# Optimization experiments

Hardware: AMD Instinct MI355X
Metric: run time of the kernel (lower is better)

Reference implementation:

```python
import jax, jax.numpy as jnp
import numpy as np

NEG_SLOPE = 0.01  # torch leaky_relu default
EPS = 1e-12      # torch F.normalize default


def _edge_mlp(edge_attr, w1, b1, w2, b2, d_h):
    # Sequential(Linear, ReLU, Linear) -> per-edge weight matrices [E, d_h, d_h]
    h = jax.nn.relu(edge_attr @ w1 + b1)
    return (h @ w2 + b2).reshape(-1, d_h, d_h)


def _nnconv(h, src, dst, w_edge, root, bias, n_nodes):
    # message_j->i = x_j @ Theta(e_ji); aggregate (add) at dst; add root transform + bias
    msg = jnp.einsum('ei,eio->eo', h[src], w_edge)  # [E, d_h]
    agg = jax.ops.segment_sum(msg, dst, num_segments=n_nodes)
    return agg + h @ root + bias


def setup_inputs() -> dict:
    key = jax.random.key(0)
    ks = jax.random.split(key, 20)
    N, E, G = 20000, 200000, 128
    d_node, d_edge, d_h, d_out = 64, 16, 32, 32

    x = jax.random.normal(ks[0], (N, d_node), dtype=jnp.float32)
    edge_index = jax.random.randint(ks[1], (2, E), 0, N, dtype=jnp.int32)
    edge_attr = jax.random.normal(ks[2], (E, d_edge), dtype=jnp.float32)
    batch = jnp.sort(jax.random.randint(ks[3], (N,), 0, G, dtype=jnp.int32))

    def lin(k, fan_in, fan_out):
        kw, kb = jax.random.split(k)
        s = 1.0 / np.sqrt(fan_in)
        w = jax.random.uniform(kw, (fan_in, fan_out), jnp.float32, -s, s)
        b = jax.random.uniform(kb, (fan_out,), jnp.float32, -s, s)
        return w, b

    nfc_w, nfc_b = lin(ks[4], d_node, d_h)
    efc1_w1, efc1_b1 = lin(ks[5], d_edge, d_h)
    efc1_w2, efc1_b2 = lin(ks[6], d_h, d_h * d_h)
    root1 = jax.random.uniform(ks[7], (d_h, d_h), jnp.float32, -1/np.sqrt(d_h), 1/np.sqrt(d_h))
    bias1 = jnp.zeros((d_h,), jnp.float32)
    efc2_w1, efc2_b1 = lin(ks[8], d_edge, d_h)
    efc2_w2, efc2_b2 = lin(ks[9], d_h, d_h * d_h)
    root2 = jax.random.uniform(ks[10], (d_h, d_h), jnp.float32, -1/np.sqrt(d_h), 1/np.sqrt(d_h))
    bias2 = jnp.zeros((d_h,), jnp.float32)
    fc_w, fc_b = lin(ks[11], d_h, d_out)

    return dict(x=x, edge_index=edge_index, edge_attr=edge_attr, batch=batch,
                num_graphs=G,
                nfc_w=nfc_w, nfc_b=nfc_b,
                efc1_w1=efc1_w1, efc1_b1=efc1_b1, efc1_w2=efc1_w2, efc1_b2=efc1_b2,
                root1=root1, bias1=bias1,
                efc2_w1=efc2_w1, efc2_b1=efc2_b1, efc2_w2=efc2_w2, efc2_b2=efc2_b2,
                root2=root2, bias2=bias2,
                fc_w=fc_w, fc_b=fc_b)


def reference(x, edge_index, edge_attr, batch, num_graphs,
              nfc_w, nfc_b,
              efc1_w1, efc1_b1, efc1_w2, efc1_b2, root1, bias1,
              efc2_w1, efc2_b1, efc2_w2, efc2_b2, root2, bias2,
              fc_w, fc_b):
    n_nodes = x.shape[0]
    d_h = nfc_w.shape[1]
    src, dst = edge_index[0], edge_index[1]

    lrelu = lambda v: jax.nn.leaky_relu(v, NEG_SLOPE)
    # dropout(p=0.1) is identity at inference
    h = lrelu(x @ nfc_w + nfc_b)

    w_e1 = _edge_mlp(edge_attr, efc1_w1, efc1_b1, efc1_w2, efc1_b2, d_h)
    h = lrelu(_nnconv(h, src, dst, w_e1, root1, bias1, n_nodes))

    w_e2 = _edge_mlp(edge_attr, efc2_w1, efc2_b1, efc2_w2, efc2_b2, d_h)
    atom_embs = lrelu(_nnconv(h, src, dst, w_e2, root2, bias2, n_nodes))

    pooled = jax.ops.segment_sum(atom_embs, batch, num_segments=num_graphs)  # [G, d_h]
    norm = jnp.linalg.norm(pooled, ord=2, axis=1, keepdims=True)
    pooled = pooled / jnp.maximum(norm, EPS)

    out = pooled @ fc_w + fc_b
    return (out, atom_embs)
```

## Files before the change

### kernel.cpp

```cpp
#include <hip/hip_runtime.h>
#include <stdint.h>

#define NN 20000
#define NE 200000
#define NG 128
#define NWJOBS 3125
#define EGRID 782
#define L2SLICE 819

typedef __attribute__((ext_vector_type(8))) short short8;
typedef __attribute__((ext_vector_type(4))) float f32x4;
typedef __attribute__((ext_vector_type(4))) int   int4v;
typedef __attribute__((ext_vector_type(2))) unsigned int uint2v;

static __device__ __forceinline__ float bf2f(short s) {
    union { unsigned int u; float f; } x;
    x.u = ((unsigned int)(unsigned short)s) << 16;
    return x.f;
}
static __device__ __forceinline__ unsigned short f2bf(float f) {
    unsigned int u = __builtin_bit_cast(unsigned int, f);
    u += 0x7fffu + ((u >> 16) & 1u);
    return (unsigned short)(u >> 16);
}
static __device__ __forceinline__ unsigned int pack2bf(float a, float b) {
    unsigned int u0 = __builtin_bit_cast(unsigned int, a) + 0x8000u;
    unsigned int u1 = __builtin_bit_cast(unsigned int, b) + 0x8000u;
    return __builtin_amdgcn_perm(u1, u0, 0x07060302u);
}
static __device__ __forceinline__ int detect_isbf(const unsigned int* x) {
    unsigned int u = x[threadIdx.x & 63];
    unsigned int el = (u >> 7) & 0xffu;
    unsigned long long bm = __ballot((el >= 100u) && (el <= 140u));
    return __popcll(bm) > 32;
}

__global__ __launch_bounds__(256) void k_prep_all(
    const void* x, const void* nfcw, const void* nfcb,
    const void* root1, const void* bias1,
    const void* w2a, const void* b2a, const void* w2b, const void* b2b,
    const void* w1a, const void* b1a, const void* w1b, const void* b1b,
    const void* ea,
    float* __restrict__ h0, float* __restrict__ aggA, float* __restrict__ aggB,
    short* __restrict__ W2Ta, short* __restrict__ W2Tb,
    short* __restrict__ w1t_ws, float* __restrict__ b1f_ws,
    short* __restrict__ ea_ws) {
    const int isbf = detect_isbf((const unsigned int*)x);
    const int b = blockIdx.x;

    if (b < 2500) {
        __shared__ float wf[64 * 32];
        __shared__ float rf[32 * 32];
        __shared__ float bfs[32];
        __shared__ float rb[32];
        __shared__ float xrow[8][66];
        __shared__ float hrow[8][33];
        for (int i = threadIdx.x; i < 64 * 32; i += 256)
            wf[i] = isbf ? bf2f(((const short*)nfcw)[i]) : ((const float*)nfcw)[i];
        for (int i = threadIdx.x; i < 32 * 32; i += 256)
            rf[i] = isbf ? bf2f(((const short*)root1)[i]) : ((const float*)root1)[i];
        if (threadIdx.x < 32) {
            bfs[threadIdx.x] = isbf ? bf2f(((const short*)nfcb)[threadIdx.x])
                                    : ((const float*)nfcb)[threadIdx.x];
            rb[threadIdx.x]  = isbf ? bf2f(((const short*)bias1)[threadIdx.x])
                                    : ((const float*)bias1)[threadIdx.x];
        }
        int t = b * 256 + threadIdx.x;
        int v = t >> 5, c = t & 31, vl = threadIdx.x >> 5;
        if (isbf) {
            const short* xr = (const short*)x + (size_t)v * 64;
            xrow[vl][c]      = bf2f(xr[c]);
            xrow[vl][32 + c] = bf2f(xr[32 + c]);
        } else {
            const float* xr = (const float*)x + (size_t)v * 64;
            xrow[vl][c]      = xr[c];
            xrow[vl][32 + c] = xr[32 + c];
        }
        __syncthreads();
        float acc = bfs[c];
#pragma unroll
        for (int q = 0; q < 64; ++q) acc += xrow[vl][q] * wf[q * 32 + c];
        float hv = acc > 0.f ? acc : 0.01f * acc;
        h0[t] = hv;
        hrow[vl][c] = hv;
        __syncthreads();
        float a2 = rb[c];
#pragma unroll
        for (int q = 0; q < 32; ++q) a2 += hrow[vl][q] * rf[q * 32 + c];
        aggA[t] = a2;
        return;
    }
    if (b < 4327) {
        const int bb = b - 2500;
        if (bb == 1) {
            for (int i = threadIdx.x; i < 1024; i += 256) {
                int layer = i >> 9, jj = i & 511, c = jj >> 4, q = jj & 15;
                const void* w1p = layer ? w1b : w1a;
                w1t_ws[i] = isbf ? ((const short*)w1p)[q * 32 + c]
                                 : (short)f2bf(((const float*)w1p)[q * 32 + c]);
            }
            for (int i = threadIdx.x; i < 64; i += 256) {
                int layer = i >> 5, c = i & 31;
                const void* b1p = layer ? b1b : b1a;
                b1f_ws[i] = isbf ? bf2f(((const short*)b1p)[c])
                                 : ((const float*)b1p)[c];
            }
        }
        int t = bb * 256 + threadIdx.x;
        if (t < 2 * 32 * 1056) {
            int layer = t / (32 * 1056);
            int r = t - layer * (32 * 1056);
            int o = r / 1056, kp = r - o * 1056;
            const void* w2 = layer ? w2b : w2a;
            const void* b2 = layer ? b2b : b2a;
            int idx; const void* sp;
            if (kp < 1024) { int kk = kp >> 5, i = kp & 31; idx = kk * 1024 + i * 32 + o; sp = w2; }
            else           { int i = kp - 1024;             idx = i * 32 + o;             sp = b2; }
            short v = isbf ? ((const short*)sp)[idx] : (short)f2bf(((const float*)sp)[idx]);
            (layer ? W2Tb : W2Ta)[o * 1056 + kp] = v;
            return;
        }
        int u = t - 2 * 32 * 1056;
        if (u < NE * 2 && !isbf) {
            const float* p = (const float*)ea + (size_t)u * 8;
            f32x4 f0 = *(const f32x4*)p;
            f32x4 f1 = *(const f32x4*)(p + 4);
            union { unsigned int d[4]; short8 v; } o8;
            o8.d[0] = pack2bf(f0[0], f0[1]);
            o8.d[1] = pack2bf(f0[2], f0[3]);
            o8.d[2] = pack2bf(f1[0], f1[1]);
            o8.d[3] = pack2bf(f1[2], f1[3]);
            *(short8*)&ea_ws[(size_t)u * 8] = o8.v;
        }
        return;
    }
    {
        int idx = (b - 4327) * 256 + threadIdx.x;
        if (idx < NN * 32 / 4) {
            f32x4 z = {0.f, 0.f, 0.f, 0.f};
            ((f32x4*)aggB)[idx] = z;
        }
    }
}

__global__ __launch_bounds__(256, 4) void k_edge(
    const float* __restrict__ h_in,
    const short* __restrict__ W2T,
    const short* __restrict__ w1pre,
    const float* __restrict__ b1pre,
    const int* __restrict__ src, const int* __restrict__ dst,
    const short* __restrict__ ea_bf,
    const short* __restrict__ ea_ws,
    const unsigned int* xdet,
    float* agg,
    const int layer2, const void* rootp, const void* biasp) {
    __shared__ __align__(16) short h1l[4 * 32 * 68];

    const int isbf = detect_isbf(xdet);
    const short* eap = isbf ? ea_bf : ea_ws;

    if (layer2) {
        const int base = blockIdx.x * L2SLICE;
        for (int i = threadIdx.x; i < L2SLICE; i += 256) {
            int t = base + i;
            if (t < NN * 32) {
                int v = t >> 5, c = t & 31;
                const float* ar = h_in + (size_t)v * 32;
                float acc = isbf ? bf2f(((const short*)biasp)[c]) : ((const float*)biasp)[c];
#pragma unroll
                for (int q = 0; q < 32; ++q) {
                    float hv = ar[q];
                    hv = hv > 0.f ? hv : 0.01f * hv;
                    float wv = isbf ? bf2f(((const short*)rootp)[q * 32 + c])
                                    : ((const float*)rootp)[q * 32 + c];
                    acc += hv * wv;
                }
                atomicAdd(&agg[t], acc);
            }
        }
    }

    const int lane = threadIdx.x & 63;
    const int wid  = threadIdx.x >> 6;
    const int m    = lane & 15;
    const int quad = lane >> 4;
    const int wb   = wid * (32 * 68);

    const int w = blockIdx.x * 4 + wid;
    if (w >= NWJOBS) return;

    short8 w1lo = {0, 0, 0, 0, 0, 0, 0, 0};
    short8 w1hi = {0, 0, 0, 0, 0, 0, 0, 0};
    if (quad < 2) {
        w1lo = *(const short8*)&w1pre[m * 16 + ((quad & 1) << 3)];
        w1hi = *(const short8*)&w1pre[(m + 16) * 16 + ((quad & 1) << 3)];
    }
    const float b1lo = b1pre[m];
    const float b1hi = b1pre[m + 16];
    const f32x4 zero4 = {0.f, 0.f, 0.f, 0.f};

    const int e0 = w << 6;
    short8 eafc[4];
    f32x4 hs[4][2];
    int4v dv[4];
    {
        int s0[4];
#pragma unroll
        for (int mt = 0; mt < 4; ++mt) {
            eafc[mt] = *(const short8*)&eap[(size_t)(e0 + mt * 16 + m) * 16 + ((quad & 1) << 3)];
            s0[mt] = src[e0 + mt * 16 + m];
            dv[mt] = *(const int4v*)&dst[e0 + mt * 16 + (quad << 2)];
        }
#pragma unroll
        for (int mt = 0; mt < 4; ++mt) {
            const float* hr = h_in + (size_t)s0[mt] * 32 + (quad << 3);
            hs[mt][0] = *(const f32x4*)hr;
            hs[mt][1] = *(const f32x4*)(hr + 4);
        }
    }

#pragma unroll
    for (int mt = 0; mt < 4; ++mt) {
        f32x4 alo = __builtin_amdgcn_mfma_f32_16x16x32_bf16(eafc[mt], w1lo, zero4, 0, 0, 0);
        f32x4 ahi = __builtin_amdgcn_mfma_f32_16x16x32_bf16(eafc[mt], w1hi, zero4, 0, 0, 0);
        float v0 = fmaxf(alo[0] + b1lo, 0.f);
        float v1 = fmaxf(alo[1] + b1lo, 0.f);
        float v2 = fmaxf(alo[2] + b1lo, 0.f);
        float v3 = fmaxf(alo[3] + b1lo, 0.f);
        uint2v dlo; dlo[0] = pack2bf(v0, v1); dlo[1] = pack2bf(v2, v3);
        *(uint2v*)&h1l[wb + m * 68 + (mt << 4) + (quad << 2)] = dlo;
        v0 = fmaxf(ahi[0] + b1hi, 0.f);
        v1 = fmaxf(ahi[1] + b1hi, 0.f);
        v2 = fmaxf(ahi[2] + b1hi, 0.f);
        v3 = fmaxf(ahi[3] + b1hi, 0.f);
        uint2v dhi; dhi[0] = pack2bf(v0, v1); dhi[1] = pack2bf(v2, v3);
        *(uint2v*)&h1l[wb + (m + 16) * 68 + (mt << 4) + (quad << 2)] = dhi;
    }
    __asm volatile("s_waitcnt lgkmcnt(0)" ::: "memory");

    short8 hsbf[4];
#pragma unroll
    for (int mt = 0; mt < 4; ++mt) {
        f32x4 g0 = hs[mt][0], g1 = hs[mt][1];
        if (layer2) {
#pragma unroll
            for (int p = 0; p < 4; ++p) {
                g0[p] = g0[p] > 0.f ? g0[p] : 0.01f * g0[p];
                g1[p] = g1[p] > 0.f ? g1[p] : 0.01f * g1[p];
            }
        }
        union { unsigned int du[4]; short8 v; } a;
        a.du[0] = pack2bf(g0[0], g0[1]);
        a.du[1] = pack2bf(g0[2], g0[3]);
        a.du[2] = pack2bf(g1[0], g1[1]);
        a.du[3] = pack2bf(g1[2], g1[3]);
        hsbf[mt] = a.v;
    }

    const short* wr0 = W2T + m * 1056 + (quad << 3);
    const short* wr1 = W2T + (m + 16) * 1056 + (quad << 3);
    f32x4 acc0[4] = {zero4, zero4, zero4, zero4};
    f32x4 acc1[4] = {zero4, zero4, zero4, zero4};
    short8 q0[4], q1[4];
#pragma unroll
    for (int p = 0; p < 4; ++p) {
        q0[p] = *(const short8*)(wr0 + (p << 5));
        q1[p] = *(const short8*)(wr1 + (p << 5));
    }
#pragma unroll
    for (int s = 0; s < 33; ++s) {
        short8 bf0 = q0[s & 3];
        short8 bf1 = q1[s & 3];
        if (s + 4 < 33) {
            q0[s & 3] = *(const short8*)(wr0 + ((s + 4) << 5));
            q1[s & 3] = *(const short8*)(wr1 + ((s + 4) << 5));
        }
        if (s < 32) {
#pragma unroll
            for (int mt = 0; mt < 4; ++mt) {
                uint2v hd = *(const uint2v*)&h1l[wb + s * 68 + (mt << 4) + (quad << 2)];
                f32x4 hv;
                hv[0] = __builtin_bit_cast(float, hd[0] << 16);
                hv[1] = __builtin_bit_cast(float, hd[0] & 0xffff0000u);
                hv[2] = __builtin_bit_cast(float, hd[1] << 16);
                hv[3] = __builtin_bit_cast(float, hd[1] & 0xffff0000u);
                f32x4 u0 = __builtin_amdgcn_mfma_f32_16x16x32_bf16(hsbf[mt], bf0, zero4, 0, 0, 0);
                f32x4 u1 = __builtin_amdgcn_mfma_f32_16x16x32_bf16(hsbf[mt], bf1, zero4, 0, 0, 0);
                acc0[mt] += hv * u0;
                acc1[mt] += hv * u1;
            }
        } else {
#pragma unroll
            for (int mt = 0; mt < 4; ++mt) {
                acc0[mt] = __builtin_amdgcn_mfma_f32_16x16x32_bf16(hsbf[mt], bf0, acc0[mt], 0, 0, 0);
                acc1[mt] = __builtin_amdgcn_mfma_f32_16x16x32_bf16(hsbf[mt], bf1, acc1[mt], 0, 0, 0);
            }
        }
    }

#pragma unroll
    for (int mt = 0; mt < 4; ++mt) {
#pragma unroll
        for (int r = 0; r < 4; ++r) {
            float* ap = agg + (size_t)dv[mt][r] * 32 + m;
            atomicAdd(ap, acc0[mt][r]);
            atomicAdd(ap + 16, acc1[mt][r]);
        }
    }
}

__global__ __launch_bounds__(256) void k_final(
    const float* __restrict__ agg, const int* __restrict__ batch,
    const unsigned int* xdet, void* __restrict__ out,
    const void* fcw, const void* fcb) {
    const int isbf = detect_isbf(xdet);
    const int g = blockIdx.x;
    __shared__ int srange[2];
    __shared__ float gacc[8][32];
    __shared__ float pn[32];
    if (threadIdx.x < 2) {
        int target = g + (int)threadIdx.x;
        int lo = 0, hi = NN;
        while (lo < hi) {
            int mid = (lo + hi) >> 1;
            if (batch[mid] < target) lo = mid + 1; else hi = mid;
        }
        srange[threadIdx.x] = lo;
    }
    __syncthreads();
    const int ns = srange[0], ne = srange[1];
    const int c = threadIdx.x & 31;
    float psum = 0.f;
    for (int idx = ns * 32 + threadIdx.x; idx < ne * 32; idx += 256) {
        float v = agg[idx];
        v = v > 0.f ? v : 0.01f * v;
        if (isbf) ((short*)out)[4096 + idx] = (short)f2bf(v);
        else      ((float*)out)[4096 + idx] = v;
        psum += v;
    }
    gacc[threadIdx.x >> 5][c] = psum;
    __syncthreads();
    if (threadIdx.x < 32) {
        float p = 0.f;
#pragma unroll
        for (int r = 0; r < 8; ++r) p += gacc[r][threadIdx.x];
        float sq = p * p;
#pragma unroll
        for (int o = 16; o > 0; o >>= 1) sq += __shfl_xor(sq, o, 64);
        float inv = 1.0f / fmaxf(sqrtf(sq), 1e-12f);
        pn[threadIdx.x] = p * inv;
    }
    __syncthreads();
    if (threadIdx.x < 32) {
        const int t = threadIdx.x;
        float acc = isbf ? bf2f(((const short*)fcb)[t]) : ((const float*)fcb)[t];
#pragma unroll
        for (int q = 0; q < 32; ++q) {
            float wv = isbf ? bf2f(((const short*)fcw)[q * 32 + t])
                            : ((const float*)fcw)[q * 32 + t];
            acc += pn[q] * wv;
        }
        if (isbf) ((short*)out)[g * 32 + t] = (short)f2bf(acc);
        else      ((float*)out)[g * 32 + t] = acc;
    }
}

extern "C" void kernel_launch(void* const* d_in, const int* in_sizes, int n_in,
                              void* d_out, int out_size, void* d_ws, size_t ws_size,
                              hipStream_t stream) {
    (void)in_sizes; (void)n_in; (void)out_size; (void)ws_size;
    const void* x     = d_in[0];
    const int*  eidx  = (const int*)d_in[1];
    const void* ea    = d_in[2];
    const int*  batch = (const int*)d_in[3];
    const void* nfcw  = d_in[5];
    const void* nfcb  = d_in[6];
    const void* e1w1  = d_in[7];
    const void* e1b1  = d_in[8];
    const void* e1w2  = d_in[9];
    const void* e1b2  = d_in[10];
    const void* root1 = d_in[11];
    const void* bias1 = d_in[12];
    const void* e2w1  = d_in[13];
    const void* e2b1  = d_in[14];
    const void* e2w2  = d_in[15];
    const void* e2b2  = d_in[16];
    const void* root2 = d_in[17];
    const void* bias2 = d_in[18];
    const void* fcw   = d_in[19];
    const void* fcb   = d_in[20];
    const unsigned int* xdet = (const unsigned int*)x;

    char* ws = (char*)d_ws;
    float* h0     = (float*)ws; ws += (size_t)NN * 32 * 4;
    float* aggA   = (float*)ws; ws += (size_t)NN * 32 * 4;
    float* aggB   = (float*)ws; ws += (size_t)NN * 32 * 4;
    short* W2T1   = (short*)ws; ws += 32 * 1056 * 2;
    short* W2T2   = (short*)ws; ws += 32 * 1056 * 2;
    short* w1t_ws = (short*)ws; ws += 1024 * 2;
    float* b1f_ws = (float*)ws; ws += 64 * 4;
    short* ea_ws  = (short*)ws; ws += (size_t)NE * 16 * 2;

    const int* srcp = eidx;
    const int* dstp = eidx + NE;

    k_prep_all<<<4952, 256, 0, stream>>>(
        x, nfcw, nfcb, root1, bias1,
        e1w2, e1b2, e2w2, e2b2, e1w1, e1b1, e2w1, e2b1, ea,
        h0, aggA, aggB, W2T1, W2T2, w1t_ws, b1f_ws, ea_ws);

    k_edge<<<EGRID, 256, 0, stream>>>(h0, W2T1, w1t_ws, b1f_ws, srcp, dstp,
                                      (const short*)ea, ea_ws, xdet, aggA,
                                      0, nullptr, nullptr);
    k_edge<<<EGRID, 256, 0, stream>>>(aggA, W2T2, w1t_ws + 512, b1f_ws + 32, srcp, dstp,
                                      (const short*)ea, ea_ws, xdet, aggB,
                                      1, root2, bias2);
    k_final<<<NG, 256, 0, stream>>>(aggB, batch, xdet, d_out, fcw, fcb);
}
```

Measured before the change: 218.5 us.

## Stage edge-MLP second-layer weights in LDS and use 1024-thread persistent blocks

The edge kernel now launches 256 blocks of 1024 threads. Each block first copies the transposed second-layer weight matrix (about 66KB in bf16) into shared memory with a padded row stride. The inner MFMA loop then reads B fragments from LDS instead of prefetching them from global or L2 memory into registers. Wave jobs are strided across blocks, and the layer-2 root transform is split into 2500-element slices per block. This cuts global weight traffic and register pressure, but it raises LDS use per block to roughly 135KB, leaves only one block per CU, adds a block-wide barrier, and wave count per block caps occupancy.

Measured after the change: 196.2 us. 10.2% less time.

```diff
diff --git a/kernel.cpp b/kernel.cpp
--- a/kernel.cpp
+++ b/kernel.cpp
@@ -5,8 +5,7 @@
 #define NE 200000
 #define NG 128
 #define NWJOBS 3125
-#define EGRID 782
-#define L2SLICE 819
+#define EBLK 256
 
 typedef __attribute__((ext_vector_type(8))) short short8;
 typedef __attribute__((ext_vector_type(4))) float f32x4;
@@ -143,7 +142,7 @@
     }
 }
 
-__global__ __launch_bounds__(256, 4) void k_edge(
+__global__ __launch_bounds__(1024, 4) void k_edge(
     const float* __restrict__ h_in,
     const short* __restrict__ W2T,
     const short* __restrict__ w1pre,
@@ -154,31 +153,35 @@
     const unsigned int* xdet,
     float* agg,
     const int layer2, const void* rootp, const void* biasp) {
-    __shared__ __align__(16) short h1l[4 * 32 * 68];
+    __shared__ __align__(16) short w2t[32 * 1058];
+    __shared__ __align__(16) short h1l[16 * 32 * 68];
 
     const int isbf = detect_isbf(xdet);
     const short* eap = isbf ? ea_bf : ea_ws;
 
+    for (int c = threadIdx.x; c < 32 * 132; c += 1024) {
+        int o = c / 132, t8 = c - o * 132;
+        *(short8*)&w2t[o * 1058 + (t8 << 3)] = *(const short8*)&W2T[o * 1056 + (t8 << 3)];
+    }
     if (layer2) {
-        const int base = blockIdx.x * L2SLICE;
-        for (int i = threadIdx.x; i < L2SLICE; i += 256) {
+        const int base = blockIdx.x * 2500;
+        for (int i = threadIdx.x; i < 2500; i += 1024) {
             int t = base + i;
-            if (t < NN * 32) {
-                int v = t >> 5, c = t & 31;
-                const float* ar = h_in + (size_t)v * 32;
-                float acc = isbf ? bf2f(((const short*)biasp)[c]) : ((const float*)biasp)[c];
-#pragma unroll
-                for (int q = 0; q < 32; ++q) {
-                    float hv = ar[q];
-                    hv = hv > 0.f ? hv : 0.01f * hv;
-                    float wv = isbf ? bf2f(((const short*)rootp)[q * 32 + c])
-                                    : ((const float*)rootp)[q * 32 + c];
-                    acc += hv * wv;
-                }
-                atomicAdd(&agg[t], acc);
-            }
-        }
-    }
+            int v = t >> 5, c = t & 31;
+            const float* ar = h_in + (size_t)v * 32;
+            float acc = isbf ? bf2f(((const short*)biasp)[c]) : ((const float*)biasp)[c];
+#pragma unroll
+            for (int q = 0; q < 32; ++q) {
+                float hv = ar[q];
+                hv = hv > 0.f ? hv : 0.01f * hv;
+                float wv = isbf ? bf2f(((const short*)rootp)[q * 32 + c])
+                                : ((const float*)rootp)[q * 32 + c];
+                acc += hv * wv;
+            }
+            atomicAdd(&agg[t], acc);
+        }
+    }
+    __syncthreads();
 
     const int lane = threadIdx.x & 63;
     const int wid  = threadIdx.x >> 6;
@@ -186,7 +189,7 @@
     const int quad = lane >> 4;
     const int wb   = wid * (32 * 68);
 
-    const int w = blockIdx.x * 4 + wid;
+    const int w = wid * EBLK + (int)blockIdx.x;
     if (w >= NWJOBS) return;
 
     short8 w1lo = {0, 0, 0, 0, 0, 0, 0, 0};
@@ -257,24 +260,12 @@
         hsbf[mt] = a.v;
     }
 
-    const short* wr0 = W2T + m * 1056 + (quad << 3);
-    const short* wr1 = W2T + (m + 16) * 1056 + (quad << 3);
     f32x4 acc0[4] = {zero4, zero4, zero4, zero4};
     f32x4 acc1[4] = {zero4, zero4, zero4, zero4};
-    short8 q0[4], q1[4];
-#pragma unroll
-    for (int p = 0; p < 4; ++p) {
-        q0[p] = *(const short8*)(wr0 + (p << 5));
-        q1[p] = *(const short8*)(wr1 + (p << 5));
-    }
 #pragma unroll
     for (int s = 0; s < 33; ++s) {
-        short8 bf0 = q0[s & 3];
-        short8 bf1 = q1[s & 3];
-        if (s + 4 < 33) {
-            q0[s & 3] = *(const short8*)(wr0 + ((s + 4) << 5));
-            q1[s & 3] = *(const short8*)(wr1 + ((s + 4) << 5));
-        }
+        short8 bf0 = *(const short8*)&w2t[m * 1058 + (s << 5) + (quad << 3)];
+        short8 bf1 = *(const short8*)&w2t[(m + 16) * 1058 + (s << 5) + (quad << 3)];
         if (s < 32) {
 #pragma unroll
             for (int mt = 0; mt < 4; ++mt) {
@@ -409,10 +400,10 @@
         e1w2, e1b2, e2w2, e2b2, e1w1, e1b1, e2w1, e2b1, ea,
         h0, aggA, aggB, W2T1, W2T2, w1t_ws, b1f_ws, ea_ws);
 
-    k_edge<<<EGRID, 256, 0, stream>>>(h0, W2T1, w1t_ws, b1f_ws, srcp, dstp,
+    k_edge<<<EBLK, 1024, 0, stream>>>(h0, W2T1, w1t_ws, b1f_ws, srcp, dstp,
                                       (const short*)ea, ea_ws, xdet, aggA,
                                       0, nullptr, nullptr);
-    k_edge<<<EGRID, 256, 0, stream>>>(aggA, W2T2, w1t_ws + 512, b1f_ws + 32, srcp, dstp,
+    k_edge<<<EBLK, 1024, 0, stream>>>(aggA, W2T2, w1t_ws + 512, b1f_ws + 32, srcp, dstp,
                                       (const short*)ea, ea_ws, xdet, aggB,
                                       1, root2, bias2);
     k_final<<<NG, 256, 0, stream>>>(aggB, batch, xdet, d_out, fcw, fcb);
```
